# Optimization experiments

Measured on AMD Instinct MI355X. Metric: run time of the kernel, lower is better.

The kernel has to match this reference:

```python
import jax, jax.numpy as jnp
import numpy as np


def setup_inputs() -> dict:
    key = jax.random.key(0)
    M, N = 2048, 16384
    x = jax.random.normal(key, (M, N), dtype=jnp.float32)
    # expk per DREAMPlace get_expk: exp(-j*pi*n/(2N)) stored as [N, 2] = (cos, -sin)
    ang = jnp.arange(N, dtype=jnp.float32) * np.float32(np.pi / (2.0 * N))
    expk = jnp.stack([jnp.cos(ang), -jnp.sin(ang)], axis=-1)
    return {"x": x, "expk": expk}


def reference(x, expk):
    """IDXCT: y_k = Re{ sum_{n=0}^{N-1} x_n * exp(j*pi/(2N) * n * (2k+1)) }.

    O(N log N) via the FFT trick:
      y_k = Re{ sum_n [x_n * exp(j*pi*n/(2N))] * exp(j*2*pi*n*k/(2N)) }
          = 2N * Re{ IFFT_{2N}(zero-padded v)[k] },  v_n = x_n * conj(expk_n)
    """
    N = x.shape[-1]
    # expk encodes exp(-j*pi*n/(2N)); we need its conjugate exp(+j*pi*n/(2N))
    v = x * (expk[..., 0] - 1j * expk[..., 1])  # complex64, [M, N]
    V = jnp.fft.ifft(v, n=2 * N, axis=-1)       # zero-padded to 2N
    y = (2 * N) * jnp.real(V[..., :N])
    return y.astype(x.dtype)
```

## Files before the change

kernel.cpp:

```cpp
#include <hip/hip_runtime.h>

constexpr int N_COLS = 16384;
constexpr int HALF   = 8192;
constexpr int NT     = 512;

__host__ __device__ constexpr int Sc(int p) {
    return p ^ ((p >> 4) & 15) ^ ((p >> 8) & 31);
}
__host__ __device__ constexpr int br4(int c) {
    return ((c & 1) << 3) | ((c & 2) << 1) | ((c & 4) >> 1) | ((c & 8) >> 3);
}

__device__ __forceinline__ void bf4(float& r0, float& i0, float& r1, float& i1,
                                    float& r2, float& i2, float& r3, float& i3,
                                    float cw, float sw) {
    float c1 = cw * cw - sw * sw;
    float s1 = 2.0f * cw * sw;
    float tr, ti;
    tr = c1 * r1 - s1 * i1; ti = c1 * i1 + s1 * r1;
    r1 = r0 - tr; i1 = i0 - ti; r0 += tr; i0 += ti;
    tr = c1 * r3 - s1 * i3; ti = c1 * i3 + s1 * r3;
    r3 = r2 - tr; i3 = i2 - ti; r2 += tr; i2 += ti;
    tr = cw * r2 - sw * i2; ti = cw * i2 + sw * r2;
    r2 = r0 - tr; i2 = i0 - ti; r0 += tr; i0 += ti;
    tr = -sw * r3 - cw * i3; ti = cw * r3 - sw * i3;
    r3 = r1 - tr; i3 = i1 - ti; r1 += tr; i1 += ti;
}

template<int SS>
__device__ __forceinline__ void round16(float2* zs, const float2* __restrict__ ek2,
                                        int sb, int j) {
    float vr[4][4], vi[4][4];
    #pragma unroll
    for (int c2 = 0; c2 < 4; ++c2)
        #pragma unroll
        for (int c1 = 0; c1 < 4; ++c1) {
            float2 v = zs[sb ^ Sc(SS * c1 + 4 * SS * c2)];
            vr[c2][c1] = v.x; vi[c2][c1] = v.y;
        }
    {
        float2 e = ek2[j * (16384 / SS)];
        float cw = e.x, sw = -e.y;
        #pragma unroll
        for (int c2 = 0; c2 < 4; ++c2)
            bf4(vr[c2][0], vi[c2][0], vr[c2][1], vi[c2][1],
                vr[c2][2], vi[c2][2], vr[c2][3], vi[c2][3], cw, sw);
    }
    #pragma unroll
    for (int c1 = 0; c1 < 4; ++c1) {
        float2 e = ek2[j * (4096 / SS) + c1 * 4096];
        bf4(vr[0][c1], vi[0][c1], vr[1][c1], vi[1][c1],
            vr[2][c1], vi[2][c1], vr[3][c1], vi[3][c1], e.x, -e.y);
    }
    #pragma unroll
    for (int c2 = 0; c2 < 4; ++c2)
        #pragma unroll
        for (int c1 = 0; c1 < 4; ++c1)
            zs[sb ^ Sc(SS * c1 + 4 * SS * c2)] = make_float2(vr[c2][c1], vi[c2][c1]);
}

__global__ __launch_bounds__(NT, 4)
void idxct_kernel(const float* __restrict__ x,
                  const float* __restrict__ expk,
                  float* __restrict__ y)
{
    __shared__ float2 zs[HALF];

    const int row = blockIdx.x;
    const float* __restrict__ xr = x + (size_t)row * N_COLS;
    float* __restrict__ yr       = y + (size_t)row * N_COLS;
    const int t   = threadIdx.x;
    const float x0 = xr[0];
    const float2* __restrict__ ek2 = (const float2*)expk;

    const int spt = Sc((int)(__brev((unsigned)t) >> 19));
    #pragma unroll
    for (int c = 0; c < 16; ++c) {
        const int k = t + NT * c;
        float2 e0 = ek2[k];
        float c0 = e0.x, s0 = -e0.y;
        float vkr, vki;
        if (c == 0 && t == 0) { vkr = x0; vki = 0.0f; }
        else {
            float a = xr[k], b = xr[N_COLS - k];
            vkr = a * c0 + b * s0;
            vki = a * s0 - b * c0;
        }
        const int K = k + HALF;
        float2 e1 = ek2[K];
        float c4 = e1.x, s4 = -e1.y;
        float a1 = xr[K], b1 = xr[N_COLS - K];
        float wkr = a1 * c4 + b1 * s4;
        float wki = a1 * s4 - b1 * c4;
        float dr = vkr - wkr, di = vki - wki;
        float cA = c0 * c0 - s0 * s0, sA = 2.0f * c0 * s0;
        float ec = cA * cA - sA * sA, es = 2.0f * cA * sA;
        float zr = (vkr + wkr) - (ec * di + es * dr);
        float zi = (vki + wki) + (ec * dr - es * di);
        zs[spt ^ br4(c)] = make_float2(zr, zi);
    }

    __syncthreads();
    round16<1>(zs, ek2, Sc(t << 4), 0);
    __syncthreads();
    round16<16>(zs, ek2, Sc(((t >> 4) << 8) | (t & 15)), t & 15);
    __syncthreads();
    round16<256>(zs, ek2, Sc(((t >> 8) << 12) | (t & 255)), t & 255);
    __syncthreads();

    {
        const int st = Sc(t);
        #pragma unroll
        for (int c = 0; c < 8; ++c) {
            const int q   = t + NT * c;
            const int sq  = st ^ Sc(NT * c);
            const int sq2 = sq ^ Sc(4096);
            float2 a = zs[sq], b = zs[sq2];
            float cw, sw;
            if (c < 4) { float2 e = ek2[q << 3];          cw = e.x; sw = -e.y; }
            else       { float2 e = ek2[(q - 2048) << 3]; cw = e.y; sw =  e.x; }
            float tr = cw * b.x - sw * b.y;
            float ti = cw * b.y + sw * b.x;
            zs[sq]  = make_float2(a.x + tr, a.y + ti);
            zs[sq2] = make_float2(a.x - tr, a.y - ti);
        }
    }
    __syncthreads();

    {
        const int st  = Sc(t);
        const int stc = Sc(t ^ 511);
        #pragma unroll
        for (int i = 0; i < 8; ++i) {
            const int m = t + NT * i;
            float2 a = zs[st  ^ Sc(NT * i)];
            float2 b = zs[stc ^ Sc((15 - i) << 9)];
            float4 o;
            o.x = 0.5f * (a.x + x0);
            o.y = 0.5f * (b.y + x0);
            o.z = 0.5f * (a.y + x0);
            o.w = 0.5f * (b.x + x0);
            *reinterpret_cast<float4*>(yr + 4 * m) = o;
        }
    }
}

extern "C" void kernel_launch(void* const* d_in, const int* in_sizes, int n_in,
                              void* d_out, int out_size, void* d_ws, size_t ws_size,
                              hipStream_t stream)
{
    const float* x    = (const float*)d_in[0];
    const float* expk = (const float*)d_in[1];
    float* y          = (float*)d_out;
    const int M = in_sizes[0] / N_COLS;
    idxct_kernel<<<dim3(M), dim3(NT), 0, stream>>>(x, expk, y);
}
```

Measured before the change: 282.3 us.

## Use 1024 threads with radix-8 register stage and fuse final butterfly into output

Doubles the block to 1024 threads and restructures the 8192-point FFT. Each thread now does a radix-8 first stage in registers before writing to LDS, followed by three radix-8 (4x2) LDS rounds. The last radix-2 stage is merged into the output pass, which removes one LDS round trip and one barrier. This trades fewer elements per thread and more waves for latency hiding against higher per-block register pressure and a different occupancy profile.

Result: slower. 293.0 us (+3.8%).

```diff
diff --git a/kernel.cpp b/kernel.cpp
--- a/kernel.cpp
+++ b/kernel.cpp
@@ -2,64 +2,74 @@
 
 constexpr int N_COLS = 16384;
 constexpr int HALF   = 8192;
-constexpr int NT     = 512;
+constexpr int NT     = 1024;
 
 __host__ __device__ constexpr int Sc(int p) {
     return p ^ ((p >> 4) & 15) ^ ((p >> 8) & 31);
 }
-__host__ __device__ constexpr int br4(int c) {
-    return ((c & 1) << 3) | ((c & 2) << 1) | ((c & 4) >> 1) | ((c & 8) >> 3);
+__host__ __device__ constexpr int br3(int c) {
+    return ((c & 1) << 2) | (c & 2) | ((c & 4) >> 2);
 }
 
-__device__ __forceinline__ void bf4(float& r0, float& i0, float& r1, float& i1,
-                                    float& r2, float& i2, float& r3, float& i3,
+__device__ __forceinline__ void bf2(float2& a, float2& b) {
+    float tr = b.x, ti = b.y;
+    b.x = a.x - tr; b.y = a.y - ti;
+    a.x += tr; a.y += ti;
+}
+__device__ __forceinline__ void bf2w(float2& a, float2& b, float cw, float sw) {
+    float tr = cw * b.x - sw * b.y;
+    float ti = cw * b.y + sw * b.x;
+    b.x = a.x - tr; b.y = a.y - ti;
+    a.x += tr; a.y += ti;
+}
+__device__ __forceinline__ void bf4(float2& e0, float2& e1, float2& e2, float2& e3,
                                     float cw, float sw) {
     float c1 = cw * cw - sw * sw;
     float s1 = 2.0f * cw * sw;
     float tr, ti;
-    tr = c1 * r1 - s1 * i1; ti = c1 * i1 + s1 * r1;
-    r1 = r0 - tr; i1 = i0 - ti; r0 += tr; i0 += ti;
-    tr = c1 * r3 - s1 * i3; ti = c1 * i3 + s1 * r3;
-    r3 = r2 - tr; i3 = i2 - ti; r2 += tr; i2 += ti;
-    tr = cw * r2 - sw * i2; ti = cw * i2 + sw * r2;
-    r2 = r0 - tr; i2 = i0 - ti; r0 += tr; i0 += ti;
-    tr = -sw * r3 - cw * i3; ti = cw * r3 - sw * i3;
-    r3 = r1 - tr; i3 = i1 - ti; r1 += tr; i1 += ti;
+    tr = c1 * e1.x - s1 * e1.y; ti = c1 * e1.y + s1 * e1.x;
+    e1.x = e0.x - tr; e1.y = e0.y - ti; e0.x += tr; e0.y += ti;
+    tr = c1 * e3.x - s1 * e3.y; ti = c1 * e3.y + s1 * e3.x;
+    e3.x = e2.x - tr; e3.y = e2.y - ti; e2.x += tr; e2.y += ti;
+    tr = cw * e2.x - sw * e2.y; ti = cw * e2.y + sw * e2.x;
+    e2.x = e0.x - tr; e2.y = e0.y - ti; e0.x += tr; e0.y += ti;
+    tr = -sw * e3.x - cw * e3.y; ti = cw * e3.x - sw * e3.y;
+    e3.x = e1.x - tr; e3.y = e1.y - ti; e1.x += tr; e1.y += ti;
 }
 
-template<int SS>
-__device__ __forceinline__ void round16(float2* zs, const float2* __restrict__ ek2,
-                                        int sb, int j) {
-    float vr[4][4], vi[4][4];
+template<int S>
+__device__ __forceinline__ void round8(float2* __restrict__ zs,
+                                       const float2* __restrict__ ek2, int t) {
+    const int j1 = t & (S - 1);
+    const int sb = Sc(((t & ~(S - 1)) << 3) | j1);
+    float2 v[2][4];
     #pragma unroll
-    for (int c2 = 0; c2 < 4; ++c2)
+    for (int c2 = 0; c2 < 2; ++c2)
         #pragma unroll
-        for (int c1 = 0; c1 < 4; ++c1) {
-            float2 v = zs[sb ^ Sc(SS * c1 + 4 * SS * c2)];
-            vr[c2][c1] = v.x; vi[c2][c1] = v.y;
-        }
+        for (int c1 = 0; c1 < 4; ++c1)
+            v[c2][c1] = zs[sb ^ Sc(S * c1 + 4 * S * c2)];
     {
-        float2 e = ek2[j * (16384 / SS)];
+        float2 e = ek2[j1 * (16384 / S)];
         float cw = e.x, sw = -e.y;
-        #pragma unroll
-        for (int c2 = 0; c2 < 4; ++c2)
-            bf4(vr[c2][0], vi[c2][0], vr[c2][1], vi[c2][1],
-                vr[c2][2], vi[c2][2], vr[c2][3], vi[c2][3], cw, sw);
+        bf4(v[0][0], v[0][1], v[0][2], v[0][3], cw, sw);
+        bf4(v[1][0], v[1][1], v[1][2], v[1][3], cw, sw);
     }
     #pragma unroll
     for (int c1 = 0; c1 < 4; ++c1) {
-        float2 e = ek2[j * (4096 / SS) + c1 * 4096];
-        bf4(vr[0][c1], vi[0][c1], vr[1][c1], vi[1][c1],
-            vr[2][c1], vi[2][c1], vr[3][c1], vi[3][c1], e.x, -e.y);
+        float2 e = ek2[j1 * (8192 / S) + (c1 & 1) * 8192];
+        float cw, sw;
+        if (c1 < 2) { cw = e.x; sw = -e.y; }
+        else        { cw = e.y; sw =  e.x; }
+        bf2w(v[0][c1], v[1][c1], cw, sw);
     }
     #pragma unroll
-    for (int c2 = 0; c2 < 4; ++c2)
+    for (int c2 = 0; c2 < 2; ++c2)
         #pragma unroll
         for (int c1 = 0; c1 < 4; ++c1)
-            zs[sb ^ Sc(SS * c1 + 4 * SS * c2)] = make_float2(vr[c2][c1], vi[c2][c1]);
+            zs[sb ^ Sc(S * c1 + 4 * S * c2)] = v[c2][c1];
 }
 
-__global__ __launch_bounds__(NT, 4)
+__global__ __launch_bounds__(NT, 8)
 void idxct_kernel(const float* __restrict__ x,
                   const float* __restrict__ expk,
                   float* __restrict__ y)
@@ -73,9 +83,9 @@
     const float x0 = xr[0];
     const float2* __restrict__ ek2 = (const float2*)expk;
 
-    const int spt = Sc((int)(__brev((unsigned)t) >> 19));
+    float2 v[8];
     #pragma unroll
-    for (int c = 0; c < 16; ++c) {
+    for (int c = 0; c < 8; ++c) {
         const int k = t + NT * c;
         float2 e0 = ek2[k];
         float c0 = e0.x, s0 = -e0.y;
@@ -95,51 +105,60 @@
         float dr = vkr - wkr, di = vki - wki;
         float cA = c0 * c0 - s0 * s0, sA = 2.0f * c0 * s0;
         float ec = cA * cA - sA * sA, es = 2.0f * cA * sA;
-        float zr = (vkr + wkr) - (ec * di + es * dr);
-        float zi = (vki + wki) + (ec * dr - es * di);
-        zs[spt ^ br4(c)] = make_float2(zr, zi);
+        v[br3(c)] = make_float2((vkr + wkr) - (ec * di + es * dr),
+                                (vki + wki) + (ec * dr - es * di));
     }
 
+    bf2(v[0], v[1]); bf2(v[2], v[3]); bf2(v[4], v[5]); bf2(v[6], v[7]);
+    bf4(v[0], v[2], v[4], v[6], 1.0f, 0.0f);
+    constexpr float RT = 0.70710678118654752440f;
+    bf4(v[1], v[3], v[5], v[7], RT, RT);
+
+    const int spb = Sc((int)(__brev((unsigned)t) >> 22) << 3);
+    #pragma unroll
+    for (int o = 0; o < 8; ++o) zs[spb ^ o] = v[o];
+
     __syncthreads();
-    round16<1>(zs, ek2, Sc(t << 4), 0);
+    round8<8>(zs, ek2, t);
     __syncthreads();
-    round16<16>(zs, ek2, Sc(((t >> 4) << 8) | (t & 15)), t & 15);
+    round8<64>(zs, ek2, t);
     __syncthreads();
-    round16<256>(zs, ek2, Sc(((t >> 8) << 12) | (t & 255)), t & 255);
+    round8<512>(zs, ek2, t);
     __syncthreads();
 
     {
-        const int st = Sc(t);
+        const int sct = Sc(t);
+        const int scr = sct ^ Sc(1023);
         #pragma unroll
-        for (int c = 0; c < 8; ++c) {
-            const int q   = t + NT * c;
-            const int sq  = st ^ Sc(NT * c);
-            const int sq2 = sq ^ Sc(4096);
-            float2 a = zs[sq], b = zs[sq2];
-            float cw, sw;
-            if (c < 4) { float2 e = ek2[q << 3];          cw = e.x; sw = -e.y; }
-            else       { float2 e = ek2[(q - 2048) << 3]; cw = e.y; sw =  e.x; }
-            float tr = cw * b.x - sw * b.y;
-            float ti = cw * b.y + sw * b.x;
-            zs[sq]  = make_float2(a.x + tr, a.y + ti);
-            zs[sq2] = make_float2(a.x - tr, a.y - ti);
-        }
-    }
-    __syncthreads();
-
-    {
-        const int st  = Sc(t);
-        const int stc = Sc(t ^ 511);
-        #pragma unroll
-        for (int i = 0; i < 8; ++i) {
-            const int m = t + NT * i;
-            float2 a = zs[st  ^ Sc(NT * i)];
-            float2 b = zs[stc ^ Sc((15 - i) << 9)];
+        for (int i = 0; i < 4; ++i) {
+            const int m  = t + NT * i;
+            const int am = sct ^ Sc(NT * i);
+            const int ar = scr ^ Sc(NT * (3 - i));
+            float2 um = zs[am];
+            float2 vm = zs[am ^ Sc(4096)];
+            float2 ur = zs[ar];
+            float2 wr = zs[ar ^ Sc(4096)];
+            float cwm, swm, cwr, swr;
+            if (i < 2) {
+                float2 e = ek2[m << 3];
+                cwm = e.x; swm = -e.y;
+                float2 f = ek2[(2047 - m) << 3];
+                cwr = f.y; swr = f.x;
+            } else {
+                float2 e = ek2[(m - 2048) << 3];
+                cwm = e.y; swm = e.x;
+                float2 f = ek2[(4095 - m) << 3];
+                cwr = f.x; swr = -f.y;
+            }
+            float trm = cwm * vm.x - swm * vm.y;
+            float tim = cwm * vm.y + swm * vm.x;
+            float trr = cwr * wr.x - swr * wr.y;
+            float tir = cwr * wr.y + swr * wr.x;
             float4 o;
-            o.x = 0.5f * (a.x + x0);
-            o.y = 0.5f * (b.y + x0);
-            o.z = 0.5f * (a.y + x0);
-            o.w = 0.5f * (b.x + x0);
+            o.x = 0.5f * ((um.x + trm) + x0);
+            o.y = 0.5f * ((ur.y - tir) + x0);
+            o.z = 0.5f * ((um.y + tim) + x0);
+            o.w = 0.5f * ((ur.x - trr) + x0);
             *reinterpret_cast<float4*>(yr + 4 * m) = o;
         }
     }
```
